# Kernel tuning notes

Hardware: AMD Instinct MI355X
Metric: run time of the kernel (lower is better)

The kernel has to match this reference:

```python
import jax, jax.numpy as jnp
import numpy as np

B, N, C_IN = 4, 48, 32
HID = [32, 32]          # hidden_channel_list
NB = [32, 32]           # neighborhood_channels
C_OUT = 16
N_BASIS = 6             # equivariant 2->2 basis ops used by SnConv2


def _masked(t, mask):
    # zero out entries for padded nodes; mask: B,n,n,n bool, t: B,n,n,n,C
    return jnp.where(mask[..., None], t, jnp.zeros((), t.dtype))


def snconv2(t, W, b):
    """Sn-equivariant 2nd-order conv on dims (1,2); dim 3 rides along.
    t: B,i,j,m,C.  W: [6, C_in, C_out], one mixing matrix per basis op."""
    n = t.shape[1]
    tT = jnp.swapaxes(t, 1, 2)                       # transpose op
    diag = jnp.einsum('biimc->bimc', t)              # diagonal, B,i,m,C
    rows = t.sum(axis=2) / n                         # row sums,  B,i,m,C
    cols = t.sum(axis=1) / n                         # col sums,  B,j,m,C
    tot = t.sum(axis=(1, 2)) / (n * n)               # total sum, B,m,C
    # contract small features BEFORE broadcasting back to 2nd order
    out = (jnp.einsum('bijmc,cd->bijmd', t, W[0])
           + jnp.einsum('bijmc,cd->bijmd', tT, W[1])
           + jnp.einsum('bimc,cd->bimd', diag, W[2])[:, :, None]
           + jnp.einsum('bimc,cd->bimd', rows, W[3])[:, :, None]
           + jnp.einsum('bjmc,cd->bjmd', cols, W[4])[:, None]
           + jnp.einsum('bmc,cd->bmd', tot, W[5])[:, None, None]
           + b)
    return out


def localconv2(t, Wv, bv, Ww, bw, Wo, bo):
    """LocalConv2, product_type='elementwise': per-channel message passing
    along the node dims: z[b,i,j] = sum_k v[b,i,k] * w[b,k,j] / n."""
    n = t.shape[1]
    v = jnp.einsum('bijmc,cd->bijmd', t, Wv) + bv
    w = jnp.einsum('bijmc,cd->bijmd', t, Ww) + bw
    z = jnp.einsum('bikmc,bkjmc->bijmc', v, w) / n
    return jnp.einsum('bijmc,cd->bijmd', z, Wo) + bo


def setup_inputs() -> dict:
    key = jax.random.key(0)
    ks = jax.random.split(key, 24)
    x = jax.random.normal(ks[0], (B, N, C_IN), dtype=jnp.float32)
    # graphs of unequal size: per-graph node counts in [N//2, N]
    sizes = jax.random.randint(ks[1], (B,), N // 2, N + 1)
    node_valid = jnp.arange(N)[None, :] < sizes[:, None]            # B,n
    mask = (node_valid[:, :, None, None]
            & node_valid[:, None, :, None]
            & node_valid[:, None, None, :])                          # B,n,n,n
    s = 0.05
    inp = {'x': x, 'mask': mask}
    cin = C_IN
    for li, (nch, cout) in enumerate(zip(NB, HID)):
        inp[f'basic_W{li}'] = s * jax.random.normal(ks[2 + 8 * li], (N_BASIS, cin, cin), dtype=jnp.float32)
        inp[f'basic_b{li}'] = jnp.zeros((cin,), jnp.float32)
        inp[f'lv_W{li}'] = s * jax.random.normal(ks[3 + 8 * li], (cin, nch), dtype=jnp.float32)
        inp[f'lv_b{li}'] = jnp.zeros((nch,), jnp.float32)
        inp[f'lw_W{li}'] = s * jax.random.normal(ks[4 + 8 * li], (cin, nch), dtype=jnp.float32)
        inp[f'lw_b{li}'] = jnp.zeros((nch,), jnp.float32)
        inp[f'lo_W{li}'] = s * jax.random.normal(ks[5 + 8 * li], (nch, cout), dtype=jnp.float32)
        inp[f'lo_b{li}'] = jnp.zeros((cout,), jnp.float32)
        cin = cout
    inp['final_W'] = s * jax.random.normal(ks[20], (N_BASIS, cin, C_OUT), dtype=jnp.float32)
    inp['final_b'] = jnp.zeros((C_OUT,), jnp.float32)
    return inp


def reference(x, mask,
              basic_W0, basic_b0, lv_W0, lv_b0, lw_W0, lw_b0, lo_W0, lo_b0,
              basic_W1, basic_b1, lv_W1, lv_b1, lw_W1, lw_b1, lo_W1, lo_b1,
              final_W, final_b):
    # order-3 outer product T[b,i,j,k,c] = x[b,i,c]*x[b,j,c]*x[b,k,c]
    t = (x[:, :, None, None, :] * x[:, None, :, None, :]) * x[:, None, None, :, :]
    t = _masked(t, mask)
    layers = [(basic_W0, basic_b0, lv_W0, lv_b0, lw_W0, lw_b0, lo_W0, lo_b0),
              (basic_W1, basic_b1, lv_W1, lv_b1, lw_W1, lw_b1, lo_W1, lo_b1)]
    for bw_, bb_, vw, vb, ww, wb, ow, ob in layers:
        t = _masked(snconv2(t, bw_, bb_), mask)
        t = localconv2(t, vw, vb, ww, wb, ow, ob)
        t = jax.nn.relu(t)
        t = _masked(t, mask)
    out = _masked(snconv2(t, final_W, final_b), mask)
    return out
```

## Files before the change

### kernel.cpp

```cpp
#include <hip/hip_runtime.h>
#include <cstdint>


namespace {

constexpr int nB = 4, nN = 48, nC = 32;
constexpr int SJ_ = nN * nC;
constexpr int SI_ = nN * SJ_;
constexpr long SB_ = (long)nN * SI_;
constexpr int RP_ = 294912;
constexpr int CP_ = 294912;
constexpr int TP_ = 6144;

__device__ __forceinline__ void decodePos(int p, int& b, int& i, int& j, int& m) {
    m = p % nN; int r = p / nN;
    j = r % nN; r /= nN;
    i = r % nN; b = r / nN;
}

__global__ __launch_bounds__(256) void k_prep(const float* __restrict__ x,
                                              const void* __restrict__ maskp,
                                              float* __restrict__ vm,
                                              float* __restrict__ S)
{
    __shared__ float vmL[nB * nN];
    const int tid = threadIdx.x;
    const unsigned int w0 = *(const unsigned int*)maskp;
    const bool is_byte = (w0 == 0x01010101u);
    if (tid < nB * nN) {
        int b = tid / nN, i = tid % nN;
        long idx = ((long)(b * nN + i) * nN + i) * nN + i;
        int bit;
        if (is_byte) bit = (((const unsigned char*)maskp)[idx] != 0);
        else         bit = (((const int*)maskp)[idx] != 0);
        float f = bit ? 1.f : 0.f;
        vm[tid] = f; vmL[tid] = f;
    }
    __syncthreads();
    if (tid < nB * nC) {
        int b = tid >> 5, c = tid & 31;
        float s = 0.f;
        for (int j = 0; j < nN; ++j) s += x[(b * nN + j) * nC + c] * vmL[b * nN + j];
        S[tid] = s;
    }
}

__global__ __launch_bounds__(256) void k_mix0(
    const float* __restrict__ x, const float* __restrict__ S,
    const float* __restrict__ Wb, const float* __restrict__ bias,
    float* __restrict__ drp, float* __restrict__ ccp, float* __restrict__ tbp)
{
    __shared__ float W2s[1024], W3s[1024], W4s[1024], W5s[1024], bs[32];
    const int tid = threadIdx.x;
    for (int q = tid; q < 1024; q += 256) {
        W2s[q] = Wb[2048 + q]; W3s[q] = Wb[3072 + q];
        W4s[q] = Wb[4096 + q]; W5s[q] = Wb[5120 + q];
    }
    if (tid < 32) bs[tid] = bias[tid];
    __syncthreads();
    const int id = blockIdx.x * 256 + tid;
    const int m = id % nN; int r = id / nN; const int i = r % nN; const int b = r / nN;
    float odr[32], occ[32];
    #pragma unroll
    for (int d = 0; d < 32; ++d) { odr[d] = 0.f; occ[d] = 0.f; }
    for (int c2 = 0; c2 < 32; ++c2) {
        float xi = x[(b * nN + i) * nC + c2];
        float xm = x[(b * nN + m) * nC + c2];
        float sc = S[b * nC + c2];
        float A = xi * xi * xm;
        float R = xi * xm * sc * (1.f / nN);
        #pragma unroll
        for (int d = 0; d < 32; ++d) {
            odr[d] = fmaf(A, W2s[c2 * 32 + d], fmaf(R, W3s[c2 * 32 + d], odr[d]));
            occ[d] = fmaf(R, W4s[c2 * 32 + d], occ[d]);
        }
    }
    #pragma unroll
    for (int d = 0; d < 32; d += 4) {
        *(float4*)(drp + (size_t)id * 32 + d) = make_float4(odr[d], odr[d+1], odr[d+2], odr[d+3]);
        *(float4*)(ccp + (size_t)id * 32 + d) = make_float4(occ[d], occ[d+1], occ[d+2], occ[d+3]);
    }
    if (i == 0) {
        float ot[32];
        #pragma unroll
        for (int d = 0; d < 32; ++d) ot[d] = bs[d];
        for (int c2 = 0; c2 < 32; ++c2) {
            float xm = x[(b * nN + m) * nC + c2];
            float sc = S[b * nC + c2];
            float Tc = xm * sc * sc * (1.f / (nN * nN));
            #pragma unroll
            for (int d = 0; d < 32; ++d) ot[d] = fmaf(Tc, W5s[c2 * 32 + d], ot[d]);
        }
        for (int d = 0; d < 32; d += 4)
            *(float4*)(tbp + (size_t)(b * nN + m) * 32 + d) = make_float4(ot[d], ot[d+1], ot[d+2], ot[d+3]);
    }
}

template <int DOUT>
__global__ __launch_bounds__(256) void k_mix(
    const float* __restrict__ dgp, const float* __restrict__ rw2,
    const float* __restrict__ cl2, const float* __restrict__ tt4,
    const float* __restrict__ Wb, const float* __restrict__ bias,
    float* __restrict__ drp, float* __restrict__ ccp, float* __restrict__ tbp)
{
    __shared__ float W2s[32 * DOUT], W3s[32 * DOUT], W4s[32 * DOUT], W5s[32 * DOUT], bs[DOUT];
    const int tid = threadIdx.x;
    for (int q = tid; q < 32 * DOUT; q += 256) {
        W2s[q] = Wb[2 * 32 * DOUT + q]; W3s[q] = Wb[3 * 32 * DOUT + q];
        W4s[q] = Wb[4 * 32 * DOUT + q]; W5s[q] = Wb[5 * 32 * DOUT + q];
    }
    if (tid < DOUT) bs[tid] = bias[tid];
    __syncthreads();
    const int id = blockIdx.x * 256 + tid;
    const int m = id % nN; int r = id / nN; const int i = r % nN; const int b = r / nN;
    float odr[DOUT], occ[DOUT];
    #pragma unroll
    for (int d = 0; d < DOUT; ++d) { odr[d] = 0.f; occ[d] = 0.f; }
    for (int c2 = 0; c2 < 32; ++c2) {
        size_t q = (size_t)id * 32 + c2;
        float dg = dgp[q];
        float rw = (rw2[q] + rw2[q + RP_]) * (1.f / nN);
        float cl = (cl2[q] + cl2[q + CP_]) * (1.f / nN);
        #pragma unroll
        for (int d = 0; d < DOUT; ++d) {
            odr[d] = fmaf(dg, W2s[c2 * DOUT + d], fmaf(rw, W3s[c2 * DOUT + d], odr[d]));
            occ[d] = fmaf(cl, W4s[c2 * DOUT + d], occ[d]);
        }
    }
    #pragma unroll
    for (int d = 0; d < DOUT; d += 4) {
        *(float4*)(drp + (size_t)id * DOUT + d) = make_float4(odr[d], odr[d+1], odr[d+2], odr[d+3]);
        *(float4*)(ccp + (size_t)id * DOUT + d) = make_float4(occ[d], occ[d+1], occ[d+2], occ[d+3]);
    }
    if (i == 0) {
        float ot[DOUT];
        #pragma unroll
        for (int d = 0; d < DOUT; ++d) ot[d] = bs[d];
        for (int c2 = 0; c2 < 32; ++c2) {
            size_t q = (size_t)(b * nN + m) * 32 + c2;
            float tv = (tt4[q] + tt4[q + TP_] + tt4[q + 2 * TP_] + tt4[q + 3 * TP_])
                       * (1.f / (nN * nN));
            #pragma unroll
            for (int d = 0; d < DOUT; ++d) ot[d] = fmaf(tv, W5s[c2 * DOUT + d], ot[d]);
        }
        for (int d = 0; d < DOUT; d += 4)
            *(float4*)(tbp + (size_t)(b * nN + m) * DOUT + d) = make_float4(ot[d], ot[d+1], ot[d+2], ot[d+3]);
    }
}

template <int MODE>
__global__ __launch_bounds__(256) void k_vw(
    const float* __restrict__ src, const float* __restrict__ vm,
    const float* __restrict__ drp, const float* __restrict__ ccp, const float* __restrict__ tbp,
    const float* __restrict__ W0, const float* __restrict__ W1,
    const float* __restrict__ Wv, const float* __restrict__ bv,
    const float* __restrict__ Ww, const float* __restrict__ bw,
    float* __restrict__ vout, float* __restrict__ wout)
{
    __shared__ float sA[128 * 34];
    __shared__ float sB[(MODE == 0) ? 64 : 128 * 34];
    const int tid = threadIdx.x;
    const long base = (long)blockIdx.x * 128;

    if (MODE == 0) {
        for (int rep = 0; rep < 4; ++rep) {
            int q = rep * 256 + tid; int pl = q >> 3, cq = q & 7;
            int p = (int)base + pl;
            int b, i, j, m; decodePos(p, b, i, j, m);
            float4 xi = *(const float4*)(src + (size_t)(b * nN + i) * nC + cq * 4);
            float4 xj = *(const float4*)(src + (size_t)(b * nN + j) * nC + cq * 4);
            float4 xm = *(const float4*)(src + (size_t)(b * nN + m) * nC + cq * 4);
            int o = pl * 34 + cq * 4;
            sA[o + 0] = xi.x * xj.x * xm.x;
            sA[o + 1] = xi.y * xj.y * xm.y;
            sA[o + 2] = xi.z * xj.z * xm.z;
            sA[o + 3] = xi.w * xj.w * xm.w;
        }
    } else {
        for (int rep = 0; rep < 4; ++rep) {
            int q = rep * 256 + tid; int pl = q >> 3, cq = q & 7;
            long p = base + pl;
            float4 a = *(const float4*)(src + p * nC + cq * 4);
            int o = pl * 34 + cq * 4;
            sA[o + 0] = a.x; sA[o + 1] = a.y; sA[o + 2] = a.z; sA[o + 3] = a.w;
            int b, i, j, m; decodePos((int)p, b, i, j, m);
            long pT = ((long)(b * nN + j) * nN + i) * nN + m;
            float4 t4 = *(const float4*)(src + pT * nC + cq * 4);
            sB[o + 0] = t4.x; sB[o + 1] = t4.y; sB[o + 2] = t4.z; sB[o + 3] = t4.w;
        }
    }
    __syncthreads();

    const int pt = tid >> 3, dq = tid & 7;
    const int p0 = pt * 4, d0 = dq * 4;
    float wc[32][4];
    float acc[4][4];

    auto zeroAcc = [&]() {
        #pragma unroll
        for (int a2 = 0; a2 < 4; ++a2)
            #pragma unroll
            for (int l = 0; l < 4; ++l) acc[a2][l] = 0.f;
    };
    auto loadW = [&](const float* Wp) {
        #pragma unroll
        for (int c2 = 0; c2 < 32; ++c2) {
            float4 q4 = *(const float4*)(Wp + c2 * nC + d0);
            wc[c2][0] = q4.x; wc[c2][1] = q4.y; wc[c2][2] = q4.z; wc[c2][3] = q4.w;
        }
    };
    auto addW = [&](const float* Wp) {
        #pragma unroll
        for (int c2 = 0; c2 < 32; ++c2) {
            float4 q4 = *(const float4*)(Wp + c2 * nC + d0);
            wc[c2][0] += q4.x; wc[c2][1] += q4.y; wc[c2][2] += q4.z; wc[c2][3] += q4.w;
        }
    };
    auto sweep = [&](const float* sp) {
        #pragma unroll
        for (int cp = 0; cp < 16; ++cp) {
            float2 t0 = *(const float2*)(sp + (p0 + 0) * 34 + cp * 2);
            float2 t1 = *(const float2*)(sp + (p0 + 1) * 34 + cp * 2);
            float2 t2 = *(const float2*)(sp + (p0 + 2) * 34 + cp * 2);
            float2 t3 = *(const float2*)(sp + (p0 + 3) * 34 + cp * 2);
            const int c0 = cp * 2, c1 = cp * 2 + 1;
            #pragma unroll
            for (int d = 0; d < 4; ++d) {
                acc[0][d] = fmaf(t0.x, wc[c0][d], acc[0][d]);
                acc[1][d] = fmaf(t1.x, wc[c0][d], acc[1][d]);
                acc[2][d] = fmaf(t2.x, wc[c0][d], acc[2][d]);
                acc[3][d] = fmaf(t3.x, wc[c0][d], acc[3][d]);
                acc[0][d] = fmaf(t0.y, wc[c1][d], acc[0][d]);
                acc[1][d] = fmaf(t1.y, wc[c1][d], acc[1][d]);
                acc[2][d] = fmaf(t2.y, wc[c1][d], acc[2][d]);
                acc[3][d] = fmaf(t3.y, wc[c1][d], acc[3][d]);
            }
        }
    };

    zeroAcc();
    if (MODE == 0) { loadW(W0); addW(W1); sweep(sA); }
    else           { loadW(W0); sweep(sA); loadW(W1); sweep(sB); }

    __syncthreads();

    #pragma unroll
    for (int l = 0; l < 4; ++l) {
        int p = (int)base + p0 + l;
        int b, i, j, m; decodePos(p, b, i, j, m);
        float4 d4 = *(const float4*)(drp + (size_t)((b * nN + i) * nN + m) * nC + d0);
        float4 c4 = *(const float4*)(ccp + (size_t)((b * nN + j) * nN + m) * nC + d0);
        float4 t4 = *(const float4*)(tbp + (size_t)(b * nN + m) * nC + d0);
        float mk = vm[b * nN + i] * vm[b * nN + j] * vm[b * nN + m];
        int o = (p0 + l) * 34 + d0;
        sA[o + 0] = (acc[l][0] + d4.x + c4.x + t4.x) * mk;
        sA[o + 1] = (acc[l][1] + d4.y + c4.y + t4.y) * mk;
        sA[o + 2] = (acc[l][2] + d4.z + c4.z + t4.z) * mk;
        sA[o + 3] = (acc[l][3] + d4.w + c4.w + t4.w) * mk;
    }
    __syncthreads();

    zeroAcc(); loadW(Wv); sweep(sA);
    {
        float4 b4 = *(const float4*)(bv + d0);
        #pragma unroll
        for (int l = 0; l < 4; ++l) {
            float4 o4 = make_float4(acc[l][0] + b4.x, acc[l][1] + b4.y,
                                    acc[l][2] + b4.z, acc[l][3] + b4.w);
            *(float4*)(vout + (size_t)(base + p0 + l) * nC + d0) = o4;
        }
    }
    zeroAcc(); loadW(Ww); sweep(sA);
    {
        float4 b4 = *(const float4*)(bw + d0);
        #pragma unroll
        for (int l = 0; l < 4; ++l) {
            float4 o4 = make_float4(acc[l][0] + b4.x, acc[l][1] + b4.y,
                                    acc[l][2] + b4.z, acc[l][3] + b4.w);
            *(float4*)(wout + (size_t)(base + p0 + l) * nC + d0) = o4;
        }
    }
}

__global__ __launch_bounds__(256, 3) void k_z(
    const float* __restrict__ v, const float* __restrict__ w,
    const float* __restrict__ Wo, const float* __restrict__ bo,
    const float* __restrict__ vm, float* __restrict__ tout,
    float* __restrict__ rows2, float* __restrict__ cols2,
    float* __restrict__ diag_, float* __restrict__ tot4)
{
    __shared__ float lds[12912];
    float* Vt = lds;
    float* Wt = lds + 6456;
    constexpr int ZS = 34;
    constexpr int ZWO = 9792;
    constexpr int TOT0 = 10816;
    const int tid = threadIdx.x;
    const int blk = blockIdx.x;
    const int tl = blk & 3; const int bm = blk >> 2;
    const int it = tl >> 1, jt = tl & 1;
    const int b = bm / nN, m = bm % nN;
    const int c = tid & 31;
    const int g = tid >> 5;
    const int i3 = g >> 1, j2 = g & 1;
    const int il0 = i3 * 6, jl0 = j2 * 12;
    const size_t posbase = (size_t)b * SB_ + (size_t)m * nC;

    float acc[6][12];
    #pragma unroll
    for (int l = 0; l < 6; ++l)
        #pragma unroll
        for (int u = 0; u < 12; ++u) acc[l][u] = 0.f;

    for (int kc = 0; kc < 6; ++kc) {
        if (kc) __syncthreads();
        #pragma unroll
        for (int rr = 0; rr < 6; ++rr) {
            int q = rr * 256 + tid; int pos = q >> 3, cq = q & 7;
            int ii = pos >> 3, kk = pos & 7;
            float4 a = *(const float4*)(v + posbase + (size_t)(it * 24 + ii) * SI_
                                          + (size_t)(kc * 8 + kk) * SJ_ + cq * 4);
            float* dst = Vt + kk * 807 + (cq * 4) * 25 + ii;
            dst[0] = a.x; dst[25] = a.y; dst[50] = a.z; dst[75] = a.w;
        }
        #pragma unroll
        for (int rr = 0; rr < 6; ++rr) {
            int q = rr * 256 + tid; int pos = q >> 3, cq = q & 7;
            int kk = pos / 24, jj = pos - kk * 24;
            float4 a = *(const float4*)(w + posbase + (size_t)(kc * 8 + kk) * SI_
                                          + (size_t)(jt * 24 + jj) * SJ_ + cq * 4);
            float* dst = Wt + kk * 807 + (cq * 4) * 25 + jj;
            dst[0] = a.x; dst[25] = a.y; dst[50] = a.z; dst[75] = a.w;
        }
        __syncthreads();
        #pragma unroll
        for (int kk = 0; kk < 8; ++kk) {
            float vf[6], wf[12];
            #pragma unroll
            for (int l = 0; l < 6; ++l) vf[l] = Vt[kk * 807 + c * 25 + il0 + l];
            #pragma unroll
            for (int u = 0; u < 12; ++u) wf[u] = Wt[kk * 807 + c * 25 + jl0 + u];
            #pragma unroll
            for (int l = 0; l < 6; ++l)
                #pragma unroll
                for (int u = 0; u < 12; ++u)
                    acc[l][u] = fmaf(vf[l], wf[u], acc[l][u]);
        }
    }
    __syncthreads();

    #pragma unroll
    for (int e = 0; e < 4; ++e)
        lds[ZWO + e * 256 + tid] = Wo[e * 256 + tid] * (1.f / nN);

    const int ptE = tid >> 3, dqE = tid & 7, d0 = dqE * 4;
    const float4 b4 = *(const float4*)(bo + d0);
    const float vmm = vm[b * nN + m];
    float colacc[3] = {0.f, 0.f, 0.f};
    float totacc = 0.f;

    for (int h = 0; h < 2; ++h) {
        if (h) __syncthreads();
        if ((i3 >> 1) == h) {
            int r0 = il0 - 12 * h;
            #pragma unroll
            for (int l = 0; l < 6; ++l)
                #pragma unroll
                for (int u = 0; u < 12; ++u)
                    lds[((r0 + l) * 24 + jl0 + u) * ZS + c] = acc[l][u];
        }
        __syncthreads();

        float oac[9][4];
        #pragma unroll
        for (int u = 0; u < 9; ++u)
            #pragma unroll
            for (int d = 0; d < 4; ++d) oac[u][d] = 0.f;
        #pragma unroll
        for (int c2 = 0; c2 < 32; ++c2) {
            float4 wo4 = *(const float4*)(lds + ZWO + c2 * 32 + d0);
            float zv[9];
            #pragma unroll
            for (int u = 0; u < 9; ++u) zv[u] = lds[(ptE * 9 + u) * ZS + c2];
            #pragma unroll
            for (int u = 0; u < 9; ++u) {
                oac[u][0] = fmaf(zv[u], wo4.x, oac[u][0]);
                oac[u][1] = fmaf(zv[u], wo4.y, oac[u][1]);
                oac[u][2] = fmaf(zv[u], wo4.z, oac[u][2]);
                oac[u][3] = fmaf(zv[u], wo4.w, oac[u][3]);
            }
        }
        __syncthreads();

        #pragma unroll
        for (int u = 0; u < 9; ++u) {
            int p = ptE * 9 + u;
            int rl = p / 24, jl = p - rl * 24;
            int gi = it * 24 + 12 * h + rl, gj = jt * 24 + jl;
            float mk = vm[b * nN + gi] * vm[b * nN + gj] * vmm;
            float4 o4;
            o4.x = fmaxf(oac[u][0] + b4.x, 0.f) * mk;
            o4.y = fmaxf(oac[u][1] + b4.y, 0.f) * mk;
            o4.z = fmaxf(oac[u][2] + b4.z, 0.f) * mk;
            o4.w = fmaxf(oac[u][3] + b4.w, 0.f) * mk;
            *(float4*)(tout + posbase + (size_t)gi * SI_ + (size_t)gj * SJ_ + d0) = o4;
            *(float2*)(lds + p * ZS + d0) = make_float2(o4.x, o4.y);
            *(float2*)(lds + p * ZS + d0 + 2) = make_float2(o4.z, o4.w);
        }
        __syncthreads();

        for (int rd = 0; rd < 2; ++rd) {
            int task = rd * 256 + tid;
            if (task < 384) {
                int i_r = task >> 5, c_r = task & 31;
                float rsum = 0.f;
                #pragma unroll
                for (int jl = 0; jl < 24; ++jl) rsum += lds[(i_r * 24 + jl) * ZS + c_r];
                int gi = it * 24 + 12 * h + i_r;
                rows2[(size_t)jt * RP_ + ((size_t)(b * nN + gi) * nN + m) * nC + c_r] = rsum;
                totacc += rsum;
                if (it == jt)
                    diag_[((size_t)(b * nN + gi) * nN + m) * nC + c_r] =
                        lds[(i_r * 24 + (12 * h + i_r)) * ZS + c_r];
            }
        }
        #pragma unroll
        for (int rr = 0; rr < 3; ++rr) {
            int task = rr * 256 + tid;
            int jl = task >> 5, c_c = task & 31;
            float csum = 0.f;
            #pragma unroll
            for (int il = 0; il < 12; ++il) csum += lds[(il * 24 + jl) * ZS + c_c];
            colacc[rr] += csum;
        }
    }

    #pragma unroll
    for (int rr = 0; rr < 3; ++rr) {
        int task = rr * 256 + tid;
        int jl = task >> 5, c_c = task & 31;
        cols2[(size_t)it * CP_ + ((size_t)(b * nN + jt * 24 + jl) * nN + m) * nC + c_c] = colacc[rr];
    }
    lds[TOT0 + g * 32 + c] = totacc;
    __syncthreads();
    if (tid < 32) {
        float s = 0.f;
        #pragma unroll
        for (int gg = 0; gg < 8; ++gg) s += lds[TOT0 + gg * 32 + tid];
        tot4[(size_t)(it * 2 + jt) * TP_ + (size_t)(b * nN + m) * nC + tid] = s;
    }
}

__global__ __launch_bounds__(256) void k_final(
    const float* __restrict__ t, const float* __restrict__ vm,
    const float* __restrict__ drp, const float* __restrict__ ccp, const float* __restrict__ tbp,
    const float* __restrict__ W0, const float* __restrict__ W1,
    float* __restrict__ out)
{
    __shared__ float sA[128 * 34], sB[128 * 34];
    const int tid = threadIdx.x;
    const long base = (long)blockIdx.x * 128;
    for (int rep = 0; rep < 4; ++rep) {
        int q = rep * 256 + tid; int pl = q >> 3, cq = q & 7;
        long p = base + pl;
        float4 a = *(const float4*)(t + p * nC + cq * 4);
        int o = pl * 34 + cq * 4;
        sA[o + 0] = a.x; sA[o + 1] = a.y; sA[o + 2] = a.z; sA[o + 3] = a.w;
        int b, i, j, m; decodePos((int)p, b, i, j, m);
        long pT = ((long)(b * nN + j) * nN + i) * nN + m;
        float4 t4 = *(const float4*)(t + pT * nC + cq * 4);
        sB[o + 0] = t4.x; sB[o + 1] = t4.y; sB[o + 2] = t4.z; sB[o + 3] = t4.w;
    }
    __syncthreads();
    const int pt = tid >> 3, dq = tid & 7;
    const int p0 = pt * 4, d0 = dq * 2;
    float wc[32][2], acc[4][2];
    #pragma unroll
    for (int l = 0; l < 4; ++l) { acc[l][0] = 0.f; acc[l][1] = 0.f; }

    auto loadW = [&](const float* Wp) {
        #pragma unroll
        for (int c2 = 0; c2 < 32; ++c2) {
            float2 q2 = *(const float2*)(Wp + c2 * 16 + d0);
            wc[c2][0] = q2.x; wc[c2][1] = q2.y;
        }
    };
    auto sweep = [&](const float* sp) {
        #pragma unroll
        for (int cp = 0; cp < 16; ++cp) {
            float2 t0 = *(const float2*)(sp + (p0 + 0) * 34 + cp * 2);
            float2 t1 = *(const float2*)(sp + (p0 + 1) * 34 + cp * 2);
            float2 t2 = *(const float2*)(sp + (p0 + 2) * 34 + cp * 2);
            float2 t3 = *(const float2*)(sp + (p0 + 3) * 34 + cp * 2);
            const int c0 = cp * 2, c1 = cp * 2 + 1;
            acc[0][0] = fmaf(t0.x, wc[c0][0], acc[0][0]); acc[0][1] = fmaf(t0.x, wc[c0][1], acc[0][1]);
            acc[1][0] = fmaf(t1.x, wc[c0][0], acc[1][0]); acc[1][1] = fmaf(t1.x, wc[c0][1], acc[1][1]);
            acc[2][0] = fmaf(t2.x, wc[c0][0], acc[2][0]); acc[2][1] = fmaf(t2.x, wc[c0][1], acc[2][1]);
            acc[3][0] = fmaf(t3.x, wc[c0][0], acc[3][0]); acc[3][1] = fmaf(t3.x, wc[c0][1], acc[3][1]);
            acc[0][0] = fmaf(t0.y, wc[c1][0], acc[0][0]); acc[0][1] = fmaf(t0.y, wc[c1][1], acc[0][1]);
            acc[1][0] = fmaf(t1.y, wc[c1][0], acc[1][0]); acc[1][1] = fmaf(t1.y, wc[c1][1], acc[1][1]);
            acc[2][0] = fmaf(t2.y, wc[c1][0], acc[2][0]); acc[2][1] = fmaf(t2.y, wc[c1][1], acc[2][1]);
            acc[3][0] = fmaf(t3.y, wc[c1][0], acc[3][0]); acc[3][1] = fmaf(t3.y, wc[c1][1], acc[3][1]);
        }
    };

    loadW(W0); sweep(sA);
    loadW(W1); sweep(sB);

    #pragma unroll
    for (int l = 0; l < 4; ++l) {
        int p = (int)base + p0 + l;
        int b, i, j, m; decodePos(p, b, i, j, m);
        float2 d2 = *(const float2*)(drp + (size_t)((b * nN + i) * nN + m) * 16 + d0);
        float2 cc2 = *(const float2*)(ccp + (size_t)((b * nN + j) * nN + m) * 16 + d0);
        float2 tb2 = *(const float2*)(tbp + (size_t)(b * nN + m) * 16 + d0);
        float mk = vm[b * nN + i] * vm[b * nN + j] * vm[b * nN + m];
        float2 o2;
        o2.x = (acc[l][0] + d2.x + cc2.x + tb2.x) * mk;
        o2.y = (acc[l][1] + d2.y + cc2.y + tb2.y) * mk;
        *(float2*)(out + (size_t)p * 16 + d0) = o2;
    }
}

}

extern "C" void kernel_launch(void* const* d_in, const int* in_sizes, int n_in,
                              void* d_out, int out_size, void* d_ws, size_t ws_size,
                              hipStream_t stream)
{
    (void)in_sizes; (void)n_in; (void)out_size; (void)ws_size;
    const float* x    = (const float*)d_in[0];
    const void*  mask = d_in[1];
    const float* bW0  = (const float*)d_in[2];
    const float* bb0  = (const float*)d_in[3];
    const float* lvW0 = (const float*)d_in[4];
    const float* lvb0 = (const float*)d_in[5];
    const float* lwW0 = (const float*)d_in[6];
    const float* lwb0 = (const float*)d_in[7];
    const float* loW0 = (const float*)d_in[8];
    const float* lob0 = (const float*)d_in[9];
    const float* bW1  = (const float*)d_in[10];
    const float* bb1  = (const float*)d_in[11];
    const float* lvW1 = (const float*)d_in[12];
    const float* lvb1 = (const float*)d_in[13];
    const float* lwW1 = (const float*)d_in[14];
    const float* lwb1 = (const float*)d_in[15];
    const float* loW1 = (const float*)d_in[16];
    const float* lob1 = (const float*)d_in[17];
    const float* fW   = (const float*)d_in[18];
    const float* fb   = (const float*)d_in[19];

    float* ws  = (float*)d_ws;
    float* t     = ws;
    float* v     = ws + 14155776L;
    float* w     = ws + 28311552L;
    float* rows2 = ws + 42467328L;
    float* cols2 = rows2 + 2 * 294912;
    float* diag  = cols2 + 2 * 294912;
    float* tot4  = diag + 294912;
    float* dr    = tot4 + 4 * 6144;
    float* cc    = dr + 294912;
    float* tb    = cc + 294912;
    float* S     = tb + 6144;
    float* vm    = S + 128;
    float* out   = (float*)d_out;

    k_prep<<<1, 256, 0, stream>>>(x, mask, vm, S);
    k_mix0<<<36, 256, 0, stream>>>(x, S, bW0, bb0, dr, cc, tb);
    k_vw<0><<<3456, 256, 0, stream>>>(x, vm, dr, cc, tb, bW0, bW0 + 1024,
                                      lvW0, lvb0, lwW0, lwb0, v, w);
    k_z<<<768, 256, 0, stream>>>(v, w, loW0, lob0, vm, t, rows2, cols2, diag, tot4);
    k_mix<32><<<36, 256, 0, stream>>>(diag, rows2, cols2, tot4, bW1, bb1, dr, cc, tb);

    k_vw<1><<<3456, 256, 0, stream>>>(t, vm, dr, cc, tb, bW1, bW1 + 1024,
                                      lvW1, lvb1, lwW1, lwb1, v, w);
    k_z<<<768, 256, 0, stream>>>(v, w, loW1, lob1, vm, t, rows2, cols2, diag, tot4);
    k_mix<16><<<36, 256, 0, stream>>>(diag, rows2, cols2, tot4, fW, fb, dr, cc, tb);
    k_final<<<3456, 256, 0, stream>>>(t, vm, dr, cc, tb, fW, fW + 512, out);
}
```

Measured before the change: 530.6 us.

## Compose SnConv2 basis weights with local v/w projections to skip intermediate pass

Precomputes products of the SnConv2 basis matrices and bias with the LocalConv2 Wv/Ww weights in a small kernel, so k_vw computes v and w directly from the input tensor without materializing the masked SnConv2 output in shared memory. The per-row/column/total mix kernels run twice, once per composed weight set, and the epilogue gathers broadcast terms separately for v and w. This removes one intermediate sweep and its barriers but doubles the gather traffic for diagonal/row/column terms and the small mix launches.

```diff
diff --git a/kernel.cpp b/kernel.cpp
--- a/kernel.cpp
+++ b/kernel.cpp
@@ -45,6 +45,37 @@
     }
 }
 
+__global__ __launch_bounds__(256) void k_compose(
+    const float* __restrict__ Wb0, const float* __restrict__ bb0,
+    const float* __restrict__ Wv0, const float* __restrict__ Ww0,
+    const float* __restrict__ Wb1, const float* __restrict__ bb1,
+    const float* __restrict__ Wv1, const float* __restrict__ Ww1,
+    float* __restrict__ cW, float* __restrict__ cb)
+{
+    const int blk = blockIdx.x;
+    const float* Wb = (blk < 2) ? Wb0 : Wb1;
+    const float* bb = (blk < 2) ? bb0 : bb1;
+    const float* Wr = (blk == 0) ? Wv0 : (blk == 1) ? Ww0 : (blk == 2) ? Wv1 : Ww1;
+    __shared__ float Ws[1024];
+    const int tid = threadIdx.x;
+    for (int q = tid; q < 1024; q += 256) Ws[q] = Wr[q];
+    __syncthreads();
+    for (int q = tid; q < 6144; q += 256) {
+        const int d = q & 31;
+        const float* row = Wb + (q >> 5) * 32;
+        float s = 0.f;
+        #pragma unroll
+        for (int e = 0; e < 32; ++e) s = fmaf(row[e], Ws[e * 32 + d], s);
+        cW[blk * 6144 + q] = s;
+    }
+    if (tid < 32) {
+        float s = 0.f;
+        #pragma unroll
+        for (int e = 0; e < 32; ++e) s = fmaf(bb[e], Ws[e * 32 + tid], s);
+        cb[blk * 32 + tid] = s;
+    }
+}
+
 __global__ __launch_bounds__(256) void k_mix0(
     const float* __restrict__ x, const float* __restrict__ S,
     const float* __restrict__ Wb, const float* __restrict__ bias,
@@ -151,10 +182,11 @@
 template <int MODE>
 __global__ __launch_bounds__(256) void k_vw(
     const float* __restrict__ src, const float* __restrict__ vm,
-    const float* __restrict__ drp, const float* __restrict__ ccp, const float* __restrict__ tbp,
-    const float* __restrict__ W0, const float* __restrict__ W1,
-    const float* __restrict__ Wv, const float* __restrict__ bv,
-    const float* __restrict__ Ww, const float* __restrict__ bw,
+    const float* __restrict__ drv, const float* __restrict__ ccv, const float* __restrict__ tbv,
+    const float* __restrict__ drw, const float* __restrict__ ccw, const float* __restrict__ tbw,
+    const float* __restrict__ WAv, const float* __restrict__ WBv,
+    const float* __restrict__ WAw, const float* __restrict__ WBw,
+    const float* __restrict__ bv, const float* __restrict__ bw,
     float* __restrict__ vout, float* __restrict__ wout)
 {
     __shared__ float sA[128 * 34];
@@ -237,49 +269,35 @@
             }
         }
     };
+    auto epilogue = [&](const float* drp, const float* ccp, const float* tbp,
+                        const float* bp, float* outp) {
+        float4 b4 = *(const float4*)(bp + d0);
+        #pragma unroll
+        for (int l = 0; l < 4; ++l) {
+            int p = (int)base + p0 + l;
+            int b, i, j, m; decodePos(p, b, i, j, m);
+            float4 d4 = *(const float4*)(drp + (size_t)((b * nN + i) * nN + m) * nC + d0);
+            float4 c4 = *(const float4*)(ccp + (size_t)((b * nN + j) * nN + m) * nC + d0);
+            float4 t4 = *(const float4*)(tbp + (size_t)(b * nN + m) * nC + d0);
+            float mk = vm[b * nN + i] * vm[b * nN + j] * vm[b * nN + m];
+            float4 o4;
+            o4.x = (acc[l][0] + d4.x + c4.x + t4.x) * mk + b4.x;
+            o4.y = (acc[l][1] + d4.y + c4.y + t4.y) * mk + b4.y;
+            o4.z = (acc[l][2] + d4.z + c4.z + t4.z) * mk + b4.z;
+            o4.w = (acc[l][3] + d4.w + c4.w + t4.w) * mk + b4.w;
+            *(float4*)(outp + (size_t)(base + p0 + l) * nC + d0) = o4;
+        }
+    };
 
     zeroAcc();
-    if (MODE == 0) { loadW(W0); addW(W1); sweep(sA); }
-    else           { loadW(W0); sweep(sA); loadW(W1); sweep(sB); }
-
-    __syncthreads();
-
-    #pragma unroll
-    for (int l = 0; l < 4; ++l) {
-        int p = (int)base + p0 + l;
-        int b, i, j, m; decodePos(p, b, i, j, m);
-        float4 d4 = *(const float4*)(drp + (size_t)((b * nN + i) * nN + m) * nC + d0);
-        float4 c4 = *(const float4*)(ccp + (size_t)((b * nN + j) * nN + m) * nC + d0);
-        float4 t4 = *(const float4*)(tbp + (size_t)(b * nN + m) * nC + d0);
-        float mk = vm[b * nN + i] * vm[b * nN + j] * vm[b * nN + m];
-        int o = (p0 + l) * 34 + d0;
-        sA[o + 0] = (acc[l][0] + d4.x + c4.x + t4.x) * mk;
-        sA[o + 1] = (acc[l][1] + d4.y + c4.y + t4.y) * mk;
-        sA[o + 2] = (acc[l][2] + d4.z + c4.z + t4.z) * mk;
-        sA[o + 3] = (acc[l][3] + d4.w + c4.w + t4.w) * mk;
-    }
-    __syncthreads();
-
-    zeroAcc(); loadW(Wv); sweep(sA);
-    {
-        float4 b4 = *(const float4*)(bv + d0);
-        #pragma unroll
-        for (int l = 0; l < 4; ++l) {
-            float4 o4 = make_float4(acc[l][0] + b4.x, acc[l][1] + b4.y,
-                                    acc[l][2] + b4.z, acc[l][3] + b4.w);
-            *(float4*)(vout + (size_t)(base + p0 + l) * nC + d0) = o4;
-        }
-    }
-    zeroAcc(); loadW(Ww); sweep(sA);
-    {
-        float4 b4 = *(const float4*)(bw + d0);
-        #pragma unroll
-        for (int l = 0; l < 4; ++l) {
-            float4 o4 = make_float4(acc[l][0] + b4.x, acc[l][1] + b4.y,
-                                    acc[l][2] + b4.z, acc[l][3] + b4.w);
-            *(float4*)(wout + (size_t)(base + p0 + l) * nC + d0) = o4;
-        }
-    }
+    if (MODE == 0) { loadW(WAv); addW(WBv); sweep(sA); }
+    else           { loadW(WAv); sweep(sA); loadW(WBv); sweep(sB); }
+    epilogue(drv, ccv, tbv, bv, vout);
+
+    zeroAcc();
+    if (MODE == 0) { loadW(WAw); addW(WBw); sweep(sA); }
+    else           { loadW(WAw); sweep(sA); loadW(WBw); sweep(sB); }
+    epilogue(drw, ccw, tbw, bw, wout);
 }
 
 __global__ __launch_bounds__(256, 3) void k_z(
@@ -558,23 +576,37 @@
     float* cols2 = rows2 + 2 * 294912;
     float* diag  = cols2 + 2 * 294912;
     float* tot4  = diag + 294912;
-    float* dr    = tot4 + 4 * 6144;
-    float* cc    = dr + 294912;
-    float* tb    = cc + 294912;
-    float* S     = tb + 6144;
+    float* drv   = tot4 + 4 * 6144;
+    float* ccv   = drv + 294912;
+    float* tbv   = ccv + 294912;
+    float* drw   = tbv + 6144;
+    float* ccw   = drw + 294912;
+    float* tbw   = ccw + 294912;
+    float* cW    = tbw + 6144;
+    float* cb    = cW + 4 * 6144;
+    float* S     = cb + 128;
     float* vm    = S + 128;
     float* out   = (float*)d_out;
 
     k_prep<<<1, 256, 0, stream>>>(x, mask, vm, S);
-    k_mix0<<<36, 256, 0, stream>>>(x, S, bW0, bb0, dr, cc, tb);
-    k_vw<0><<<3456, 256, 0, stream>>>(x, vm, dr, cc, tb, bW0, bW0 + 1024,
-                                      lvW0, lvb0, lwW0, lwb0, v, w);
+    k_compose<<<4, 256, 0, stream>>>(bW0, bb0, lvW0, lwW0, bW1, bb1, lvW1, lwW1, cW, cb);
+
+    k_mix0<<<36, 256, 0, stream>>>(x, S, cW + 0,    cb + 0,  drv, ccv, tbv);
+    k_mix0<<<36, 256, 0, stream>>>(x, S, cW + 6144, cb + 32, drw, ccw, tbw);
+    k_vw<0><<<3456, 256, 0, stream>>>(x, vm, drv, ccv, tbv, drw, ccw, tbw,
+                                      cW + 0,    cW + 1024,
+                                      cW + 6144, cW + 7168,
+                                      lvb0, lwb0, v, w);
     k_z<<<768, 256, 0, stream>>>(v, w, loW0, lob0, vm, t, rows2, cols2, diag, tot4);
-    k_mix<32><<<36, 256, 0, stream>>>(diag, rows2, cols2, tot4, bW1, bb1, dr, cc, tb);
-
-    k_vw<1><<<3456, 256, 0, stream>>>(t, vm, dr, cc, tb, bW1, bW1 + 1024,
-                                      lvW1, lvb1, lwW1, lwb1, v, w);
+
+    k_mix<32><<<36, 256, 0, stream>>>(diag, rows2, cols2, tot4, cW + 12288, cb + 64, drv, ccv, tbv);
+    k_mix<32><<<36, 256, 0, stream>>>(diag, rows2, cols2, tot4, cW + 18432, cb + 96, drw, ccw, tbw);
+    k_vw<1><<<3456, 256, 0, stream>>>(t, vm, drv, ccv, tbv, drw, ccw, tbw,
+                                      cW + 12288, cW + 13312,
+                                      cW + 18432, cW + 19456,
+                                      lvb1, lwb1, v, w);
     k_z<<<768, 256, 0, stream>>>(v, w, loW1, lob1, vm, t, rows2, cols2, diag, tot4);
-    k_mix<16><<<36, 256, 0, stream>>>(diag, rows2, cols2, tot4, fW, fb, dr, cc, tb);
-    k_final<<<3456, 256, 0, stream>>>(t, vm, dr, cc, tb, fW, fW + 512, out);
-}
+
+    k_mix<16><<<36, 256, 0, stream>>>(diag, rows2, cols2, tot4, fW, fb, drv, ccv, tbv);
+    k_final<<<3456, 256, 0, stream>>>(t, vm, drv, ccv, tbv, fW, fW + 512, out);
+}
```

Measured after the change: 724.9 us. 36.6% more time.
